# Kernel tuning notes

Measured on AMD Instinct MI355X. Metric: run time of the kernel, lower is better.

Reference implementation:

```python
import jax, jax.numpy as jnp
import numpy as np

D_MODEL = 1024
N_HEADS = 16
HEAD_DIM = D_MODEL // N_HEADS
B, T = 4, 2048


def setup_inputs() -> dict:
    key = jax.random.key(0)
    k_x, k_len, k_wqkv, k_bqkv, k_wo, k_bo = jax.random.split(key, 6)
    x = jax.random.normal(k_x, (B, T, D_MODEL), dtype=jnp.float32)
    # left-aligned valid-token mask: first `length` tokens valid per sequence
    lengths = jax.random.randint(k_len, (B,), T // 2, T + 1)
    attention_mask = (jnp.arange(T)[None, :] < lengths[:, None]).astype(jnp.int32)
    s = 1.0 / np.sqrt(D_MODEL)
    Wqkv = jax.random.normal(k_wqkv, (3 * D_MODEL, D_MODEL), dtype=jnp.float32) * s
    bqkv = jax.random.normal(k_bqkv, (3 * D_MODEL,), dtype=jnp.float32) * 0.01
    Wo = jax.random.normal(k_wo, (D_MODEL, D_MODEL), dtype=jnp.float32) * s
    bo = jax.random.normal(k_bo, (D_MODEL,), dtype=jnp.float32) * 0.01
    return {"x": x, "attention_mask": attention_mask,
            "Wqkv": Wqkv, "bqkv": bqkv, "Wo": Wo, "bo": bo}


def reference(x, attention_mask, Wqkv, bqkv, Wo, bo):
    Bx, Tx, C = x.shape
    qkv = x @ Wqkv.T + bqkv                      # [B,T,3C]
    q, k, v = jnp.split(qkv, 3, axis=-1)
    def heads(t):                                # [B,T,C] -> [B,H,T,hd]
        return t.reshape(Bx, Tx, N_HEADS, HEAD_DIM).transpose(0, 2, 1, 3)
    q, k, v = heads(q), heads(k), heads(v)
    att = jnp.einsum('bhqd,bhkd->bhqk', q, k) / np.sqrt(HEAD_DIM)
    causal = jnp.tril(jnp.ones((Tx, Tx), dtype=bool))[None, None]
    att = jnp.where(causal, att, -jnp.inf)
    key_mask = attention_mask.astype(bool)[:, None, None, :]  # [B,1,1,T]
    att = jnp.where(key_mask, att, -jnp.inf)
    att = jax.nn.softmax(att, axis=-1)
    query_mask = attention_mask.astype(att.dtype)[:, None, :, None]
    att = att * query_mask
    y = jnp.einsum('bhqk,bhkd->bhqd', att, v)
    y = y.transpose(0, 2, 1, 3).reshape(Bx, Tx, C)
    y = y * attention_mask.astype(y.dtype)[:, :, None]
    return y @ Wo.T + bo
```

## Files before the change

### kernel.cpp

```cpp
#include <hip/hip_runtime.h>
#include <hip/hip_bf16.h>
#include <stdint.h>
#include <math.h>

#define D_MODEL 1024
#define N_HEADS 16
#define HEAD_DIM 64
#define BB 4
#define TT 2048
#define M_TOK (BB * TT)

typedef __attribute__((ext_vector_type(8))) short short8;
typedef __attribute__((ext_vector_type(4))) short short4v;
typedef __attribute__((ext_vector_type(4))) float float4v;

#define KS_STRIDE 72
#define VT_STRIDE 76

#define QK_SCALE 0.18033688011f

__device__ __forceinline__ short f2bf(float f) {
    union { float f; uint32_t u; } v; v.f = f;
    uint32_t u = v.u;
    uint32_t r = u + 0x7FFF + ((u >> 16) & 1);
    return (short)(r >> 16);
}
__device__ __forceinline__ float bf2f(short s) {
    union { uint32_t u; float f; } v;
    v.u = ((uint32_t)(unsigned short)s) << 16;
    return v.f;
}

__device__ __forceinline__ float exp2fast(float x) {
#if __has_builtin(__builtin_amdgcn_exp2f)
    return __builtin_amdgcn_exp2f(x);
#else
    return exp2f(x);
#endif
}

__device__ __forceinline__ uint32_t pktrunc(float hi, float lo) {
    return __builtin_amdgcn_perm(__builtin_bit_cast(uint32_t, hi),
                                 __builtin_bit_cast(uint32_t, lo),
                                 0x07060302u);
}

__device__ __forceinline__ float4v mfma16(short4v a, short4v b, float4v c) {
#if __has_builtin(__builtin_amdgcn_mfma_f32_16x16x16bf16_1k)
    return __builtin_amdgcn_mfma_f32_16x16x16bf16_1k(a, b, c, 0, 0, 0);
#else
    asm volatile("v_mfma_f32_16x16x16_bf16 %0, %1, %2, %0"
                 : "+v"(c) : "v"(a), "v"(b));
    return c;
#endif
}
__device__ __forceinline__ float4v mfma32(short8 a, short8 b, float4v c) {
    return __builtin_amdgcn_mfma_f32_16x16x32_bf16(a, b, c, 0, 0, 0);
}

__device__ __forceinline__ void async_cp16(const short* g, short* l) {
    __builtin_amdgcn_global_load_lds(
        (const __attribute__((address_space(1))) void*)g,
        (__attribute__((address_space(3))) void*)l, 16, 0, 0);
}

__global__ void probe_kernel(const unsigned short* __restrict__ xs,
                             const int* __restrict__ mask,
                             int* __restrict__ flag) {
    __shared__ int red[256];
    const int tid = threadIdx.x;
    const int task = blockIdx.x;
    if (task == 0) {
        int cnt = 0;
        for (int i = tid; i < 8192; i += 256) {
            const unsigned short u = xs[i];
            if (((u >> 7) & 0xFF) >= 134) cnt++;
        }
        red[tid] = cnt;
        __syncthreads();
        for (int s = 128; s > 0; s >>= 1) {
            if (tid < s) red[tid] += red[tid + s];
            __syncthreads();
        }
        if (tid == 0) flag[0] = (red[0] > 512) ? 1 : 0;
    } else {
        const int b = task - 1;
        int c = 0;
        for (int i = tid; i < TT; i += 256) c += (mask[b * TT + i] != 0) ? 1 : 0;
        red[tid] = c;
        __syncthreads();
        for (int s = 128; s > 0; s >>= 1) {
            if (tid < s) red[tid] += red[tid + s];
            __syncthreads();
        }
        if (tid == 0) flag[4 + b] = red[0];
    }
}

__global__ __launch_bounds__(256) void cvt_kernel(
    const void* __restrict__ src, short* __restrict__ dst,
    const int* __restrict__ flag, int n8) {
    const int i = blockIdx.x * 256 + threadIdx.x;
    if (i >= n8) return;
    if (*flag) {
        const float4v f0 = ((const float4v*)src)[2 * i];
        const float4v f1 = ((const float4v*)src)[2 * i + 1];
        short8 o;
        for (int j = 0; j < 4; ++j) { o[j] = f2bf(f0[j]); o[j + 4] = f2bf(f1[j]); }
        ((short8*)dst)[i] = o;
    } else {
        ((short8*)dst)[i] = ((const short8*)src)[i];
    }
}

__global__ __launch_bounds__(256) void gemm_qkv(
    const short* __restrict__ X, const short* __restrict__ W,
    const void* __restrict__ biasv, void* __restrict__ outv,
    const int* __restrict__ flagp, int M, int N, int K) {
    __shared__ short As[128 * 32];
    __shared__ short Bs[128 * 32];

    const int f32m = flagp[0];
    const int bm = blockIdx.y * 128;
    const int bn = blockIdx.x * 128;
    const int len = flagp[4 + (bm >> 11)];
    if ((bm & (TT - 1)) >= len) return;

    const int tid  = threadIdx.x;
    const int lane = tid & 63;
    const int wave = tid >> 6;
    const int quad = lane >> 4;
    const int l16  = lane & 15;
    const int wm = (wave >> 1) * 64;
    const int wn = (wave & 1) * 64;

    float4v acc[4][4];
    const float4v zero4 = {0.f, 0.f, 0.f, 0.f};
    for (int i = 0; i < 4; ++i)
        for (int j = 0; j < 4; ++j) acc[i][j] = zero4;

    const int srow = tid >> 2;
    const int skc  = (tid & 3) * 8;
    const short* xg0 = &X[(size_t)(bm + srow) * K + skc];
    const short* xg1 = &X[(size_t)(bm + 64 + srow) * K + skc];
    const short* wg0 = &W[(size_t)(bn + srow) * K + skc];
    const short* wg1 = &W[(size_t)(bn + 64 + srow) * K + skc];
    short* asd0 = &As[wave * 512];
    short* asd1 = &As[2048 + wave * 512];
    short* bsd0 = &Bs[wave * 512];
    short* bsd1 = &Bs[2048 + wave * 512];

    for (int k0 = 0; k0 < K; k0 += 32) {
        __syncthreads();
        async_cp16(xg0 + k0, asd0);
        async_cp16(xg1 + k0, asd1);
        async_cp16(wg0 + k0, bsd0);
        async_cp16(wg1 + k0, bsd1);
        __syncthreads();

        short8 a[4], b[4];
        for (int i = 0; i < 4; ++i)
            a[i] = *(short8*)&As[(wm + i * 16 + l16) * 32 + quad * 8];
        for (int j = 0; j < 4; ++j)
            b[j] = *(short8*)&Bs[(wn + j * 16 + l16) * 32 + quad * 8];
        for (int i = 0; i < 4; ++i)
            for (int j = 0; j < 4; ++j)
                acc[i][j] = __builtin_amdgcn_mfma_f32_16x16x32_bf16(
                    a[i], b[j], acc[i][j], 0, 0, 0);
    }

    const bool vblock = (bn >= 2 * D_MODEL);
    for (int i = 0; i < 4; ++i) {
        for (int j = 0; j < 4; ++j) {
            const int n = bn + wn + j * 16 + l16;
            const float bf = f32m ? ((const float*)biasv)[n]
                                  : bf2f(((const short*)biasv)[n]);
            if (vblock) {
                const int t0 = bm + wm + i * 16 + quad * 4;
                const int b  = t0 >> 11;
                const int t  = t0 & (TT - 1);
                const int hh = (n >> 6) & 15;
                const int d  = n & 63;
                short4v pk;
                for (int r = 0; r < 4; ++r) pk[r] = f2bf(acc[i][j][r] + bf);
                short* dst = (short*)outv + 2 * (size_t)BB * N_HEADS * TT * HEAD_DIM;
                *(short4v*)&dst[(((size_t)b * N_HEADS + hh) * HEAD_DIM + d) * TT + t] = pk;
                continue;
            }
            const int wh = n >> 10;
            const float scale = (wh == 0) ? QK_SCALE : 1.0f;
            for (int r = 0; r < 4; ++r) {
                const int m = bm + wm + i * 16 + quad * 4 + r;
                const int b  = m >> 11;
                const int t  = m & (TT - 1);
                const int hh = (n >> 6) & 15;
                const int d  = n & 63;
                short* dst = (short*)outv +
                    (size_t)wh * ((size_t)BB * N_HEADS * TT * HEAD_DIM);
                dst[(((size_t)b * N_HEADS + hh) * TT + t) * HEAD_DIM + d] =
                    f2bf((acc[i][j][r] + bf) * scale);
            }
        }
    }
}

__global__ __launch_bounds__(256) void gemm_out(
    const short* __restrict__ X, const short* __restrict__ W,
    const void* __restrict__ biasv, void* __restrict__ outv,
    const int* __restrict__ flagp, int M, int N, int K) {
    __shared__ short As[64 * 32];
    __shared__ short Bs[128 * 32];
    __shared__ float Es[4][16][66];

    const int f32m = flagp[0];
    const int bm = blockIdx.y * 64;
    const int bn = blockIdx.x * 128;
    const int len = flagp[4 + (bm >> 11)];
    const bool dead = (bm & (TT - 1)) >= len;

    const int tid  = threadIdx.x;
    const int lane = tid & 63;
    const int wave = tid >> 6;
    const int quad = lane >> 4;
    const int l16  = lane & 15;
    const int wm = (wave >> 1) * 32;
    const int wn = (wave & 1) * 64;

    float4v acc[2][4];
    const float4v zero4 = {0.f, 0.f, 0.f, 0.f};
    for (int i = 0; i < 2; ++i)
        for (int j = 0; j < 4; ++j) acc[i][j] = zero4;

    if (!dead) {
        const int srow = tid >> 2;
        const int skc  = (tid & 3) * 8;
        const short* xg  = &X[(size_t)(bm + srow) * K + skc];
        const short* wg0 = &W[(size_t)(bn + srow) * K + skc];
        const short* wg1 = &W[(size_t)(bn + 64 + srow) * K + skc];
        short* asd  = &As[wave * 512];
        short* bsd0 = &Bs[wave * 512];
        short* bsd1 = &Bs[2048 + wave * 512];

        for (int k0 = 0; k0 < K; k0 += 32) {
            __syncthreads();
            async_cp16(xg + k0, asd);
            async_cp16(wg0 + k0, bsd0);
            async_cp16(wg1 + k0, bsd1);
            __syncthreads();

            short8 a[2], b[4];
            for (int i = 0; i < 2; ++i)
                a[i] = *(short8*)&As[(wm + i * 16 + l16) * 32 + quad * 8];
            for (int j = 0; j < 4; ++j)
                b[j] = *(short8*)&Bs[(wn + j * 16 + l16) * 32 + quad * 8];
            for (int i = 0; i < 2; ++i)
                for (int j = 0; j < 4; ++j)
                    acc[i][j] = __builtin_amdgcn_mfma_f32_16x16x32_bf16(
                        a[i], b[j], acc[i][j], 0, 0, 0);
        }
    }

    for (int i = 0; i < 2; ++i) {
        for (int j = 0; j < 4; ++j) {
            const int n = bn + wn + j * 16 + l16;
            const float bf = f32m ? ((const float*)biasv)[n]
                                  : bf2f(((const short*)biasv)[n]);
            for (int r = 0; r < 4; ++r)
                Es[wave][quad * 4 + r][j * 16 + l16] =
                    dead ? bf : (acc[i][j][r] + bf);
        }
        for (int pass = 0; pass < 4; ++pass) {
            const int row = pass * 4 + quad;
            const int m = bm + wm + i * 16 + row;
            const float4v v4 = *(float4v*)&Es[wave][row][l16 * 4];
            const size_t off = (size_t)m * N + bn + wn + l16 * 4;
            if (f32m) {
                *(float4v*)&((float*)outv)[off] = v4;
            } else {
                short4v pk;
                for (int r = 0; r < 4; ++r) pk[r] = f2bf(v4[r]);
                *(short4v*)&((short*)outv)[off] = pk;
            }
        }
    }
}

__global__ __launch_bounds__(256) void attn_kernel(
    const short* __restrict__ Q, const short* __restrict__ Kb,
    const short* __restrict__ Vt_g, const int* __restrict__ flagp,
    short* __restrict__ Y) {
    __shared__ short Ks[2][64 * KS_STRIDE];
    __shared__ short Vt[2][64 * VT_STRIDE];

    const int x = blockIdx.x;
    const int h = blockIdx.y, b = blockIdx.z;
    const int tid  = threadIdx.x;
    const int lane = tid & 63;
    const int wave = tid >> 6;
    const int quad = lane >> 4;
    const int l16  = lane & 15;

    const int len = flagp[4 + b];
    const int L64 = (len + 63) >> 6;
    const size_t bh = ((size_t)b * N_HEADS + h) * TT * HEAD_DIM;

    const int cA = x;
    const int cB = L64 - 1 - x;
    const bool pair = (cB >= cA);
    const bool hasB = (cB > cA);

    if (pair) {
        const int qwA = cA * 64 + wave * 16;
        const int qwB = cB * 64 + wave * 16;

        short8 qa[2][2];
        for (int c = 0; c < 2; ++c)
            qa[0][c] = *(const short8*)&Q[bh + (size_t)(qwA + l16) * HEAD_DIM + c * 32 + quad * 8];
        if (hasB)
            for (int c = 0; c < 2; ++c)
                qa[1][c] = *(const short8*)&Q[bh + (size_t)(qwB + l16) * HEAD_DIM + c * 32 + quad * 8];

        const float4v zero4 = {0.f, 0.f, 0.f, 0.f};
        const short one_bf = (short)0x3F80;
        const short8 ones8 = {one_bf, one_bf, one_bf, one_bf,
                              one_bf, one_bf, one_bf, one_bf};
        float4v o[2][4];
        for (int qf = 0; qf < 2; ++qf)
            for (int i = 0; i < 4; ++i) o[qf][i] = zero4;
        float4v ps[2] = {zero4, zero4};

        const int srow = tid >> 2;
        const int scol = (tid & 3) * 16;

        short8 kr0, kr1, vr0, vr1;
#define LOAD_TILE(kb)                                                     \
        {                                                                 \
            const size_t gk = bh + (size_t)((kb) + srow) * HEAD_DIM + scol;\
            const size_t gv = bh + (size_t)srow * TT + (kb) + scol;       \
            kr0 = *(const short8*)&Kb[gk];   kr1 = *(const short8*)&Kb[gk + 8];\
            vr0 = *(const short8*)&Vt_g[gv]; vr1 = *(const short8*)&Vt_g[gv + 8];\
        }
#define STORE_TILE(buf)                                                   \
        {                                                                 \
            *(short8*)&Ks[buf][srow * KS_STRIDE + scol]     = kr0;        \
            *(short8*)&Ks[buf][srow * KS_STRIDE + scol + 8] = kr1;        \
            *(short8*)&Vt[buf][srow * VT_STRIDE + scol]     = vr0;        \
            *(short8*)&Vt[buf][srow * VT_STRIDE + scol + 8] = vr1;        \
        }

        const int ntiles = cB + 1;
        LOAD_TILE(0);
        STORE_TILE(0);
        if (ntiles > 1) LOAD_TILE(64);
        __syncthreads();

        for (int kt = 0; kt < ntiles; ++kt) {
            const int kbase = kt * 64;
            const int cur = kt & 1;
            if (kt + 1 < ntiles) {
                STORE_TILE(1 - cur);
                if (kt + 2 < ntiles) LOAD_TILE(kbase + 128);
            }

            const int qmaxw = (hasB ? qwB : qwA) + 15;
            if (kbase <= qmaxw) {
                short8 kbf[4][2];
                for (int nt = 0; nt < 4; ++nt) {
                    kbf[nt][0] = *(short8*)&Ks[cur][(nt * 16 + l16) * KS_STRIDE + quad * 8];
                    kbf[nt][1] = *(short8*)&Ks[cur][(nt * 16 + l16) * KS_STRIDE + 32 + quad * 8];
                }
#pragma unroll
                for (int qf = 0; qf < 2; ++qf) {
                    if (qf == 1 && !hasB) continue;
                    const int qw = qf ? qwB : qwA;
                    if (kbase > qw + 15) continue;

                    float4v s[4];
                    for (int nt = 0; nt < 4; ++nt) {
                        float4v z = zero4;
                        z = mfma32(kbf[nt][0], qa[qf][0], z);
                        z = mfma32(kbf[nt][1], qa[qf][1], z);
                        s[nt] = z;
                    }

                    const int q = qw + l16;
                    float ev[4][4];
                    const bool full = (kbase + 63 <= qw) && (kbase + 64 <= len);
                    if (full) {
#pragma unroll
                        for (int nt = 0; nt < 4; ++nt)
                            for (int r = 0; r < 4; ++r)
                                ev[nt][r] = exp2fast(s[nt][r]);
                    } else {
#pragma unroll
                        for (int nt = 0; nt < 4; ++nt)
                            for (int r = 0; r < 4; ++r) {
                                const int key = kbase + nt * 16 + quad * 4 + r;
                                const float e = exp2fast(s[nt][r]);
                                ev[nt][r] = (key <= q && key < len) ? e : 0.f;
                            }
                    }

                    union { uint32_t u[4]; short8 v; } P0, P1;
                    P0.u[0] = pktrunc(ev[0][1], ev[0][0]);
                    P0.u[1] = pktrunc(ev[0][3], ev[0][2]);
                    P0.u[2] = pktrunc(ev[1][1], ev[1][0]);
                    P0.u[3] = pktrunc(ev[1][3], ev[1][2]);
                    P1.u[0] = pktrunc(ev[2][1], ev[2][0]);
                    P1.u[1] = pktrunc(ev[2][3], ev[2][2]);
                    P1.u[2] = pktrunc(ev[3][1], ev[3][0]);
                    P1.u[3] = pktrunc(ev[3][3], ev[3][2]);

                    ps[qf] = mfma32(P0.v, ones8, ps[qf]);
                    ps[qf] = mfma32(P1.v, ones8, ps[qf]);

                    union { uint32_t u[2]; short4v v; } pf[4];
                    pf[0].u[0] = P0.u[0]; pf[0].u[1] = P0.u[1];
                    pf[1].u[0] = P0.u[2]; pf[1].u[1] = P0.u[3];
                    pf[2].u[0] = P1.u[0]; pf[2].u[1] = P1.u[1];
                    pf[3].u[0] = P1.u[2]; pf[3].u[1] = P1.u[3];

                    for (int nt2 = 0; nt2 < 4; ++nt2) {
                        float4v accv = o[qf][nt2];
                        for (int nt = 0; nt < 4; ++nt) {
                            short4v vf = *(short4v*)&Vt[cur][(nt2 * 16 + l16) * VT_STRIDE
                                                             + nt * 16 + quad * 4];
                            accv = mfma16(pf[nt].v, vf, accv);
                        }
                        o[qf][nt2] = accv;
                    }
                }
            }
            __syncthreads();
        }
#undef LOAD_TILE
#undef STORE_TILE

#pragma unroll
        for (int qf = 0; qf < 2; ++qf) {
            if (qf == 1 && !hasB) continue;
            const int qw = qf ? qwB : qwA;
            for (int r = 0; r < 4; ++r) {
                const int q = qw + quad * 4 + r;
                const float denom = ps[qf][r];
                const float inv = (denom > 0.f && q < len)
                                      ? __builtin_amdgcn_rcpf(denom) : 0.f;
                for (int nt2 = 0; nt2 < 4; ++nt2) {
                    Y[((size_t)(b * TT + q)) * D_MODEL + h * HEAD_DIM + nt2 * 16 + l16] =
                        f2bf(o[qf][nt2][r] * inv);
                }
            }
        }
    }

    const int z = 31 - x;
    if (z >= L64) {
        const short4v zz = {0, 0, 0, 0};
        for (int r = 0; r < 4; ++r) {
            const int q = z * 64 + wave * 16 + quad * 4 + r;
            *(short4v*)&Y[((size_t)(b * TT + q)) * D_MODEL + h * HEAD_DIM + l16 * 4] = zz;
        }
    }
}

extern "C" void kernel_launch(void* const* d_in, const int* in_sizes, int n_in,
                              void* d_out, int out_size, void* d_ws, size_t ws_size,
                              hipStream_t stream) {
    const void* x    = d_in[0];
    const int*  mask = (const int*)d_in[1];
    const void* Wqkv = d_in[2];
    const void* bqkv = d_in[3];
    const void* Wo   = d_in[4];
    const void* bo   = d_in[5];

    int*   flag = (int*)d_ws;
    short* qbuf = (short*)d_ws + 128;
    const size_t QSZ = (size_t)BB * N_HEADS * TT * HEAD_DIM;
    short* kbuf = qbuf + QSZ;
    short* vbuf = qbuf + 2 * QSZ;
    short* xyb  = qbuf + 3 * QSZ;
    short* wqb  = qbuf + 4 * QSZ;

    probe_kernel<<<5, 256, 0, stream>>>((const unsigned short*)x, mask, flag);

    cvt_kernel<<<(M_TOK * D_MODEL / 8 + 255) / 256, 256, 0, stream>>>(
        x, xyb, flag, M_TOK * D_MODEL / 8);
    cvt_kernel<<<(3 * D_MODEL * D_MODEL / 8 + 255) / 256, 256, 0, stream>>>(
        Wqkv, wqb, flag, 3 * D_MODEL * D_MODEL / 8);

    gemm_qkv<<<dim3((3 * D_MODEL) / 128, M_TOK / 128), 256, 0, stream>>>(
        xyb, wqb, bqkv, qbuf, flag, M_TOK, 3 * D_MODEL, D_MODEL);

    attn_kernel<<<dim3(16, N_HEADS, BB), 256, 0, stream>>>(
        qbuf, kbuf, vbuf, flag, xyb);

    cvt_kernel<<<(D_MODEL * D_MODEL / 8 + 255) / 256, 256, 0, stream>>>(
        Wo, kbuf, flag, D_MODEL * D_MODEL / 8);

    gemm_out<<<dim3(D_MODEL / 128, M_TOK / 64), 256, 0, stream>>>(
        xyb, kbuf, bo, d_out, flag, M_TOK, D_MODEL, D_MODEL);
}
```

Measured before the change: 291.9 us.

## Share V fragments across paired query chunks and remap blocks for XCD locality

Blocks are remapped from a linearized grid ID so that consecutive IDs, which are dispatched round-robin across the eight XCDs, place the two heads sharing an XCD together. This aims to improve L2 reuse of K and V per XCD. The PV stage now processes both query chunks in one loop, so each V fragment read from LDS feeds two MFMAs instead of being loaded twice. This raises register pressure, and the remap hardcodes the grid shape (16x16x4).

Result: no change. 291.8 us (-0.0%).

```diff
diff --git a/kernel.cpp b/kernel.cpp
--- a/kernel.cpp
+++ b/kernel.cpp
@@ -292,8 +292,13 @@
     __shared__ short Ks[2][64 * KS_STRIDE];
     __shared__ short Vt[2][64 * VT_STRIDE];
 
-    const int x = blockIdx.x;
-    const int h = blockIdx.y, b = blockIdx.z;
+    const int g   = blockIdx.x + 16 * blockIdx.y + 256 * blockIdx.z;
+    const int xcd = g & 7;
+    const int sub = g >> 3;
+    const int x   = sub >> 3;
+    const int b   = sub & 3;
+    const int h   = (xcd << 1) | ((sub >> 2) & 1);
+
     const int tid  = threadIdx.x;
     const int lane = tid & 63;
     const int wave = tid >> 6;
@@ -349,6 +354,7 @@
         }
 
         const int ntiles = cB + 1;
+        const int qmaxw = (hasB ? qwB : qwA) + 15;
         LOAD_TILE(0);
         STORE_TILE(0);
         if (ntiles > 1) LOAD_TILE(64);
@@ -362,27 +368,29 @@
                 if (kt + 2 < ntiles) LOAD_TILE(kbase + 128);
             }
 
-            const int qmaxw = (hasB ? qwB : qwA) + 15;
             if (kbase <= qmaxw) {
                 short8 kbf[4][2];
+#pragma unroll
                 for (int nt = 0; nt < 4; ++nt) {
                     kbf[nt][0] = *(short8*)&Ks[cur][(nt * 16 + l16) * KS_STRIDE + quad * 8];
                     kbf[nt][1] = *(short8*)&Ks[cur][(nt * 16 + l16) * KS_STRIDE + 32 + quad * 8];
                 }
-#pragma unroll
-                for (int qf = 0; qf < 2; ++qf) {
-                    if (qf == 1 && !hasB) continue;
-                    const int qw = qf ? qwB : qwA;
-                    if (kbase > qw + 15) continue;
-
+                const bool doA = (kbase <= qwA + 15);
+                const bool doB = hasB;
+
+                union pfu { uint32_t u[2]; short4v v; };
+                pfu pfA[4], pfB[4];
+
+                auto do_chunk = [&](const short8* qaf, const int qw,
+                                    float4v& psa, pfu* pf) {
                     float4v s[4];
+#pragma unroll
                     for (int nt = 0; nt < 4; ++nt) {
                         float4v z = zero4;
-                        z = mfma32(kbf[nt][0], qa[qf][0], z);
-                        z = mfma32(kbf[nt][1], qa[qf][1], z);
+                        z = mfma32(kbf[nt][0], qaf[0], z);
+                        z = mfma32(kbf[nt][1], qaf[1], z);
                         s[nt] = z;
                     }
-
                     const int q = qw + l16;
                     float ev[4][4];
                     const bool full = (kbase + 63 <= qw) && (kbase + 64 <= len);
@@ -400,7 +408,6 @@
                                 ev[nt][r] = (key <= q && key < len) ? e : 0.f;
                             }
                     }
-
                     union { uint32_t u[4]; short8 v; } P0, P1;
                     P0.u[0] = pktrunc(ev[0][1], ev[0][0]);
                     P0.u[1] = pktrunc(ev[0][3], ev[0][2]);
@@ -410,21 +417,41 @@
                     P1.u[1] = pktrunc(ev[2][3], ev[2][2]);
                     P1.u[2] = pktrunc(ev[3][1], ev[3][0]);
                     P1.u[3] = pktrunc(ev[3][3], ev[3][2]);
-
-                    ps[qf] = mfma32(P0.v, ones8, ps[qf]);
-                    ps[qf] = mfma32(P1.v, ones8, ps[qf]);
-
-                    union { uint32_t u[2]; short4v v; } pf[4];
+                    psa = mfma32(P0.v, ones8, psa);
+                    psa = mfma32(P1.v, ones8, psa);
                     pf[0].u[0] = P0.u[0]; pf[0].u[1] = P0.u[1];
                     pf[1].u[0] = P0.u[2]; pf[1].u[1] = P0.u[3];
                     pf[2].u[0] = P1.u[0]; pf[2].u[1] = P1.u[1];
                     pf[3].u[0] = P1.u[2]; pf[3].u[1] = P1.u[3];
-
+                };
+                if (doA) do_chunk(qa[0], qwA, ps[0], pfA);
+                if (doB) do_chunk(qa[1], qwB, ps[1], pfB);
+
+                if (doA && doB) {
+#pragma unroll
+                    for (int nt2 = 0; nt2 < 4; ++nt2) {
+                        float4v aA = o[0][nt2];
+                        float4v aB = o[1][nt2];
+#pragma unroll
+                        for (int nt = 0; nt < 4; ++nt) {
+                            const short4v vf = *(short4v*)&Vt[cur][(nt2 * 16 + l16) * VT_STRIDE
+                                                                   + nt * 16 + quad * 4];
+                            aA = mfma16(pfA[nt].v, vf, aA);
+                            aB = mfma16(pfB[nt].v, vf, aB);
+                        }
+                        o[0][nt2] = aA;
+                        o[1][nt2] = aB;
+                    }
+                } else {
+                    const pfu* pf = doA ? pfA : pfB;
+                    const int qf = doA ? 0 : 1;
+#pragma unroll
                     for (int nt2 = 0; nt2 < 4; ++nt2) {
                         float4v accv = o[qf][nt2];
+#pragma unroll
                         for (int nt = 0; nt < 4; ++nt) {
-                            short4v vf = *(short4v*)&Vt[cur][(nt2 * 16 + l16) * VT_STRIDE
-                                                             + nt * 16 + quad * 4];
+                            const short4v vf = *(short4v*)&Vt[cur][(nt2 * 16 + l16) * VT_STRIDE
+                                                                   + nt * 16 + quad * 4];
                             accv = mfma16(pf[nt].v, vf, accv);
                         }
                         o[qf][nt2] = accv;
```
